# Optimization experiments

Measured on AMD Instinct MI355X. Metric: run time of the kernel, lower is better.

Reference implementation:

```python
import jax, jax.numpy as jnp
import numpy as np

B, S, HID = 8, 1024, 1024
NH, HD = 16, 64  # num heads, head dim
EPS = 1e-12


def setup_inputs() -> dict:
    key = jax.random.key(0)
    ks = jax.random.split(key, 8)
    sc = 0.02
    return {
        "hidden_states": jax.random.normal(ks[0], (B, S, HID), jnp.float32),
        "attention_mask": jnp.zeros((B, 1, 1, S), jnp.bool_),
        "rel_pos": jax.random.normal(ks[1], (1, NH, S, S), jnp.float32),
        "rel_2d_pos": jax.random.normal(ks[2], (1, NH, S, S), jnp.float32),
        "w_qkv": jax.random.normal(ks[3], (3 * HID, HID), jnp.float32) * sc,
        "q_bias": jnp.zeros((1, 1, HID), jnp.float32),
        "v_bias": jnp.zeros((1, 1, HID), jnp.float32),
        "w_out": jax.random.normal(ks[4], (HID, HID), jnp.float32) * sc,
        "b_out": jnp.zeros((HID,), jnp.float32),
        "ln_gamma": jnp.ones((HID,), jnp.float32),
        "ln_beta": jnp.zeros((HID,), jnp.float32),
    }


def reference(hidden_states, attention_mask, rel_pos, rel_2d_pos,
              w_qkv, q_bias, v_bias, w_out, b_out, ln_gamma, ln_beta):
    x = hidden_states
    # fast_qkv: single projection, no bias; then add q_bias/v_bias
    qkv = jnp.einsum('bsh,oh->bso', x, w_qkv)  # [B,S,3*HID]
    q, k, v = jnp.split(qkv, 3, axis=-1)
    q = q + q_bias
    v = v + v_bias
    # [B,S,HID] -> [B,NH,S,HD]
    to_heads = lambda t: t.reshape(B, S, NH, HD).transpose(0, 2, 1, 3)
    qh, kh, vh = to_heads(q), to_heads(k), to_heads(v)
    qh = qh / jnp.sqrt(jnp.float32(HD))
    scores = jnp.einsum('bhqd,bhkd->bhqk', qh, kh)
    scores = scores + rel_pos + rel_2d_pos
    scores = jnp.where(attention_mask, -jnp.inf, scores.astype(jnp.float32))
    probs = jax.nn.softmax(scores, axis=-1).astype(vh.dtype)
    ctx = jnp.einsum('bhqk,bhkd->bhqd', probs, vh)
    ctx = ctx.transpose(0, 2, 1, 3).reshape(B, S, HID)
    # self-output: dense + residual + LayerNorm
    h = jnp.einsum('bsh,oh->bso', ctx, w_out) + b_out + x
    mu = jnp.mean(h, axis=-1, keepdims=True)
    var = jnp.var(h, axis=-1, keepdims=True)
    out = (h - mu) / jnp.sqrt(var + EPS) * ln_gamma + ln_beta
    return out
```

## Files before the change

kernel.cpp:

```cpp
#include <hip/hip_runtime.h>
#include <stdint.h>
#include <stddef.h>

typedef unsigned short u16;
typedef __attribute__((ext_vector_type(8))) short short8;
typedef __attribute__((ext_vector_type(4))) float f32x4;
typedef __attribute__((ext_vector_type(4))) unsigned short ushort4v;
typedef __attribute__((ext_vector_type(4))) unsigned char uchar4v;
typedef __attribute__((ext_vector_type(2))) unsigned int uint2v;

constexpr int B_ = 8, S_ = 1024, HID_ = 1024, NH_ = 16, HD_ = 64;
#define LOG2E_F 1.4426950408889634f
#define QSCALE_F 0.18033688011112043f
#define SHIFT2_F 11.541560327111707f

__device__ __forceinline__ u16 f2b(float f) {
  unsigned int u = __builtin_bit_cast(unsigned int, f);
  u += 0x7fff + ((u >> 16) & 1);
  return (u16)(u >> 16);
}
__device__ __forceinline__ float b2f(u16 s) {
  unsigned int u = ((unsigned int)s) << 16;
  return __builtin_bit_cast(float, u);
}
__device__ __forceinline__ float fexp2(float x) {
#if __has_builtin(__builtin_amdgcn_exp2f)
  return __builtin_amdgcn_exp2f(x);
#else
  return exp2f(x);
#endif
}
__device__ __forceinline__ void llds16(const void* g, void* l) {
  __builtin_amdgcn_global_load_lds((__attribute__((address_space(1))) void*)g,
                                   (__attribute__((address_space(3))) void*)l, 16, 0, 0);
}

__global__ __launch_bounds__(256) void prep_cvt(
    const float* __restrict__ x, const float* __restrict__ wqkv,
    const float* __restrict__ wout, u16* __restrict__ xb,
    u16* __restrict__ wqkvb, u16* __restrict__ woutb) {
  const int NX4 = B_ * S_ * HID_ / 4, NW14 = 3 * HID_ * HID_ / 4, NW24 = HID_ * HID_ / 4;
  const int tot = NX4 + NW14 + NW24;
  for (int i = blockIdx.x * blockDim.x + threadIdx.x; i < tot; i += gridDim.x * blockDim.x) {
    const float4* s; u16* d; int j;
    if (i < NX4)              { s = (const float4*)x;    d = xb;    j = i; }
    else if (i < NX4 + NW14)  { s = (const float4*)wqkv; d = wqkvb; j = i - NX4; }
    else                      { s = (const float4*)wout; d = woutb; j = i - NX4 - NW14; }
    float4 v = s[j];
    ushort4v o; o[0] = f2b(v.x); o[1] = f2b(v.y); o[2] = f2b(v.z); o[3] = f2b(v.w);
    *(ushort4v*)(d + 4 * (size_t)j) = o;
  }
}

__global__ __launch_bounds__(256) void rel_perm(
    const float* __restrict__ a, const float* __restrict__ b, u16* __restrict__ relb) {
  __shared__ u16 lbuf[16 * 1032];
  const int qtg = blockIdx.x, h = blockIdx.y;
  const int t = threadIdx.x;
#pragma unroll
  for (int it = 0; it < 16; ++it) {
    int idx = it * 256 + t;
    int lq = idx >> 8, kc = idx & 255;
    size_t src = ((size_t)h * S_ + qtg * 16 + lq) * S_ + kc * 4;
    float4 va = *(const float4*)(a + src);
    float4 vb = *(const float4*)(b + src);
    ushort4v o;
    o[0] = f2b((va.x + vb.x) * LOG2E_F); o[1] = f2b((va.y + vb.y) * LOG2E_F);
    o[2] = f2b((va.z + vb.z) * LOG2E_F); o[3] = f2b((va.w + vb.w) * LOG2E_F);
    *(ushort4v*)(lbuf + lq * 1032 + kc * 4) = o;
  }
  __syncthreads();
#pragma unroll
  for (int it = 0; it < 16; ++it) {
    int c = it * 16 + (t >> 4);
    int ktg = c >> 2, qk = c & 3, lq = t & 15;
    ushort4v v = *(const ushort4v*)(lbuf + lq * 1032 + ktg * 16 + qk * 4);
    *(ushort4v*)(relb + ((((size_t)h * 64 + ktg) * 64 + qtg) * 4 + qk) * 64 + lq * 4) = v;
  }
}

__global__ __launch_bounds__(256) void gemm_qkv(
    const u16* __restrict__ W, const u16* __restrict__ X,
    const float* __restrict__ qbias, const float* __restrict__ vbias,
    u16* __restrict__ Qb, u16* __restrict__ Kb, u16* __restrict__ Vtb) {
  constexpr int K = HID_;
  __shared__ u16 smem[128 * 136];
  u16* Ws0 = smem;
  u16* Ws1 = smem + 4096;
  u16* Xs0 = smem + 8192;
  u16* Xs1 = smem + 12288;
  const int lin = blockIdx.x;
  const int virt = (lin & 7) * 192 + (lin >> 3);
  const int o0 = (virt % 24) * 128, s0 = (virt / 24) * 128;
  const int t = threadIdx.x, lane = t & 63, wv = t >> 6;
  const int wr = wv >> 1, wc = wv & 1, ln = lane & 15, q8 = lane >> 4;
  f32x4 acc[4][4] = {};

  for (int kt = 0; kt < K / 64; ++kt) {
    const int k0 = kt * 64;
#pragma unroll
    for (int c = 0; c < 2; ++c) {
      int idx = c * 256 + t, row = idx >> 2, cc = (idx & 3) * 8;
      const int db = (c * 256 + wv * 64) * 8;
      llds16(W + (size_t)(o0 + row) * K + k0 + cc,      Ws0 + db);
      llds16(W + (size_t)(o0 + row) * K + k0 + 32 + cc, Ws1 + db);
      llds16(X + (size_t)(s0 + row) * K + k0 + cc,      Xs0 + db);
      llds16(X + (size_t)(s0 + row) * K + k0 + 32 + cc, Xs1 + db);
    }
    __syncthreads();
#pragma unroll
    for (int hh = 0; hh < 2; ++hh) {
      const u16* Wh = hh ? Ws1 : Ws0;
      const u16* Xh = hh ? Xs1 : Xs0;
      short8 of[4], sf[4];
#pragma unroll
      for (int mi = 0; mi < 4; ++mi)
        of[mi] = *(const short8*)(Wh + (wr * 64 + mi * 16 + ln) * 32 + q8 * 8);
#pragma unroll
      for (int ni = 0; ni < 4; ++ni)
        sf[ni] = *(const short8*)(Xh + (wc * 64 + ni * 16 + ln) * 32 + q8 * 8);
#pragma unroll
      for (int mi = 0; mi < 4; ++mi)
#pragma unroll
        for (int ni = 0; ni < 4; ++ni)
          acc[mi][ni] = __builtin_amdgcn_mfma_f32_16x16x32_bf16(of[mi], sf[ni], acc[mi][ni], 0, 0, 0);
    }
    __syncthreads();
  }

  const int sec = o0 >> 10;

  if (sec == 2) {
#pragma unroll
    for (int mi = 0; mi < 4; ++mi) {
      const int ocol = wr * 64 + mi * 16 + q8 * 4;
      const int oo = (o0 + ocol) & 1023;
      float4 b4 = *(const float4*)(vbias + oo);
#pragma unroll
      for (int ni = 0; ni < 4; ++ni) {
        const int srow = wc * 64 + ni * 16 + ln;
#pragma unroll
        for (int r = 0; r < 4; ++r)
          smem[(ocol + r) * 136 + srow] = f2b(acc[mi][ni][r] + ((const float*)&b4)[r]);
      }
    }
    __syncthreads();
#pragma unroll
    for (int i = 0; i < 8; ++i) {
      int flat = i * 256 + t;
      int dl = flat >> 4, s8 = (flat & 15) * 8;
      short8 v = *(const short8*)(smem + dl * 136 + s8);
      int oo = (o0 + dl) & 1023, hh = oo >> 6, dd = oo & 63;
      int bb = s0 >> 10, ss = (s0 + s8) & 1023;
      *(short8*)(Vtb + ((size_t)(bb * NH_ + hh) * HD_ + dd) * S_ + ss) = v;
    }
    return;
  }

#pragma unroll
  for (int mi = 0; mi < 4; ++mi) {
    const int ocol = wr * 64 + mi * 16 + q8 * 4;
    const int oo = (o0 + ocol) & 1023;
    float4 b4;
    if (sec == 0) b4 = *(const float4*)(qbias + oo);
    else          b4 = float4{0.f, 0.f, 0.f, 0.f};
#pragma unroll
    for (int ni = 0; ni < 4; ++ni) {
      const int srow = wc * 64 + ni * 16 + ln;
      u16 e[4];
#pragma unroll
      for (int r = 0; r < 4; ++r) {
        float v = acc[mi][ni][r] + ((const float*)&b4)[r];
        if (sec == 0) v *= QSCALE_F;
        e[r] = f2b(v);
      }
      uint2v pw;
      pw[0] = (unsigned)e[0] | ((unsigned)e[1] << 16);
      pw[1] = (unsigned)e[2] | ((unsigned)e[3] << 16);
      *(uint2v*)(smem + srow * 136 + ocol) = pw;
    }
  }
  __syncthreads();
  u16* dst = (sec == 0) ? Qb : Kb;
#pragma unroll
  for (int i = 0; i < 8; ++i) {
    int flat = i * 256 + t;
    int srow = flat >> 4, c8 = (flat & 15) * 8;
    short8 v = *(const short8*)(smem + srow * 136 + c8);
    int oo = (o0 + c8) & 1023, hh = oo >> 6, dd = oo & 63;
    int s = s0 + srow, bb = s >> 10, ss = s & 1023;
    *(short8*)(dst + ((size_t)(bb * NH_ + hh) * S_ + ss) * HD_ + dd) = v;
  }
}

__global__ __launch_bounds__(512, 2) void flash_attn(
    const u16* __restrict__ Qb, const u16* __restrict__ Kb,
    const u16* __restrict__ Vtb, const u16* __restrict__ relb,
    const unsigned char* __restrict__ mask, u16* __restrict__ ctxb) {
  const int lin = blockIdx.x;
  const int virt = (lin & 7) * 64 + (lin >> 3);
  const int h = virt >> 5, qt_blk = (virt >> 3) & 3, b = virt & 7;
  const int bh = b * NH_ + h, q0 = qt_blk * 256;
  const int t = threadIdx.x, lane = t & 63, wv = t >> 6;
  const int ln = lane & 15, q8 = lane >> 4;

  __shared__ u16 smem[28160];
  u16* Ks  = smem;
  u16* Vts = smem + 9216;
  u16* Pw  = smem + 17920 + wv * 1280;

  const int krow = t >> 3, kcol = (t & 7) * 8;
  const int vrow = t >> 4, vcol = (t & 15) * 8;

  const u16* relbase = relb + (((size_t)h * 64) * 64 + (size_t)(qt_blk * 16 + wv * 2)) * 4 * 64
                            + (size_t)q8 * 64 + ln * 4;

  short8 kreg[2], vreg[2];
#pragma unroll
  for (int i = 0; i < 2; ++i)
    kreg[i] = *(const short8*)(Kb + ((size_t)bh * S_ + i * 64 + krow) * HD_ + kcol);
#pragma unroll
  for (int i = 0; i < 2; ++i)
    vreg[i] = *(const short8*)(Vtb + ((size_t)bh * HD_ + i * 32 + vrow) * S_ + vcol);

  short8 qf[2][2];
#pragma unroll
  for (int qt = 0; qt < 2; ++qt)
#pragma unroll
    for (int kc = 0; kc < 2; ++kc)
      qf[qt][kc] = *(const short8*)(Qb + ((size_t)bh * S_ + q0 + wv * 32 + qt * 16 + ln) * HD_ + kc * 32 + q8 * 8);

  f32x4 Oa[4][2] = {};
  float rs2[2] = {0.f, 0.f};

  for (int kt128 = 0; kt128 < 8; ++kt128) {
    const int k0 = kt128 * 128;

    uchar4v mg[4][2];
#pragma unroll
    for (int kvc = 0; kvc < 4; ++kvc)
#pragma unroll
      for (int sub = 0; sub < 2; ++sub)
        mg[kvc][sub] = *(const uchar4v*)(mask + b * S_ + k0 + (kvc * 2 + sub) * 16 + q8 * 4);

    ushort4v relg[4][2][2];
#pragma unroll
    for (int sub = 0; sub < 2; ++sub)
#pragma unroll
      for (int qt = 0; qt < 2; ++qt)
        relg[0][sub][qt] = *(const ushort4v*)(relbase +
            (((size_t)(kt128 * 8 + sub) * 64 + qt) * 4) * 64);

    __syncthreads();
#pragma unroll
    for (int i = 0; i < 2; ++i)
      *(short8*)(Ks + (i * 64 + krow) * 72 + kcol) = kreg[i];
#pragma unroll
    for (int i = 0; i < 2; ++i)
      *(short8*)(Vts + (i * 32 + vrow) * 136 + vcol) = vreg[i];
    if (kt128 < 7) {
      const int k0n = k0 + 128;
#pragma unroll
      for (int i = 0; i < 2; ++i)
        kreg[i] = *(const short8*)(Kb + ((size_t)bh * S_ + k0n + i * 64 + krow) * HD_ + kcol);
#pragma unroll
      for (int i = 0; i < 2; ++i)
        vreg[i] = *(const short8*)(Vtb + ((size_t)bh * HD_ + i * 32 + vrow) * S_ + k0n + vcol);
    }
    __syncthreads();

#pragma unroll
    for (int kvc = 0; kvc < 4; ++kvc) {
      if (kvc < 3) {
#pragma unroll
        for (int sub = 0; sub < 2; ++sub)
#pragma unroll
          for (int qt = 0; qt < 2; ++qt)
            relg[kvc + 1][sub][qt] = *(const ushort4v*)(relbase +
                (((size_t)(kt128 * 8 + (kvc + 1) * 2 + sub) * 64 + qt) * 4) * 64);
      }
#pragma unroll
      for (int sub = 0; sub < 2; ++sub) {
        const int kt = kvc * 2 + sub;
        short8 kf0 = *(const short8*)(Ks + (kt * 16 + ln) * 72 + q8 * 8);
        short8 kf1 = *(const short8*)(Ks + (kt * 16 + ln) * 72 + 32 + q8 * 8);
        uchar4v m4 = mg[kvc][sub];
        f32x4 mbase;
#pragma unroll
        for (int r = 0; r < 4; ++r) mbase[r] = (m4[r] ? -1e30f : 0.f) - SHIFT2_F;
#pragma unroll
        for (int qt = 0; qt < 2; ++qt) {
          ushort4v r4 = relg[kvc][sub][qt];
          f32x4 sc;
#pragma unroll
          for (int r = 0; r < 4; ++r) sc[r] = b2f(r4[r]) + mbase[r];
          sc = __builtin_amdgcn_mfma_f32_16x16x32_bf16(kf0, qf[qt][0], sc, 0, 0, 0);
          sc = __builtin_amdgcn_mfma_f32_16x16x32_bf16(kf1, qf[qt][1], sc, 0, 0, 0);
          float p0 = fexp2(sc[0]), p1 = fexp2(sc[1]);
          float p2 = fexp2(sc[2]), p3 = fexp2(sc[3]);
          rs2[qt] += (p0 + p1) + (p2 + p3);
          uint2v pw;
          pw[0] = (unsigned)f2b(p0) | ((unsigned)f2b(p1) << 16);
          pw[1] = (unsigned)f2b(p2) | ((unsigned)f2b(p3) << 16);
          *(uint2v*)(Pw + (qt * 16 + ln) * 40 + sub * 16 + q8 * 4) = pw;
        }
      }
      short8 pf0 = *(const short8*)(Pw + ln * 40 + q8 * 8);
      short8 pf1 = *(const short8*)(Pw + (16 + ln) * 40 + q8 * 8);
#pragma unroll
      for (int mt = 0; mt < 4; ++mt) {
        short8 vf = *(const short8*)(Vts + (mt * 16 + ln) * 136 + kvc * 32 + q8 * 8);
        Oa[mt][0] = __builtin_amdgcn_mfma_f32_16x16x32_bf16(vf, pf0, Oa[mt][0], 0, 0, 0);
        Oa[mt][1] = __builtin_amdgcn_mfma_f32_16x16x32_bf16(vf, pf1, Oa[mt][1], 0, 0, 0);
      }
    }
  }

  float inv[2];
#pragma unroll
  for (int qt = 0; qt < 2; ++qt) {
    rs2[qt] += __shfl_xor(rs2[qt], 16, 64);
    rs2[qt] += __shfl_xor(rs2[qt], 32, 64);
    inv[qt] = 1.f / rs2[qt];
  }

  __syncthreads();
  u16* Ob = smem + wv * 2304;
#pragma unroll
  for (int qt = 0; qt < 2; ++qt)
#pragma unroll
    for (int mt = 0; mt < 4; ++mt) {
      u16 e[4];
#pragma unroll
      for (int r = 0; r < 4; ++r) e[r] = f2b(Oa[mt][qt][r] * inv[qt]);
      uint2v pw;
      pw[0] = (unsigned)e[0] | ((unsigned)e[1] << 16);
      pw[1] = (unsigned)e[2] | ((unsigned)e[3] << 16);
      *(uint2v*)(Ob + (qt * 16 + ln) * 72 + mt * 16 + q8 * 4) = pw;
    }
#pragma unroll
  for (int p = 0; p < 4; ++p) {
    int row = p * 8 + (lane >> 3);
    int c8 = (lane & 7) * 8;
    short8 v = *(const short8*)(Ob + row * 72 + c8);
    int q = q0 + wv * 32 + row;
    *(short8*)(ctxb + ((size_t)(b * S_ + q)) * HID_ + h * 64 + c8) = v;
  }
}

__global__ __launch_bounds__(256) void gemm_out(
    const u16* __restrict__ W, const u16* __restrict__ X,
    const float* __restrict__ bout, const float* __restrict__ xres,
    u16* __restrict__ hb) {
  constexpr int K = HID_;
  __shared__ u16 smem[128 * 136];
  u16* Ws0 = smem;
  u16* Ws1 = smem + 4096;
  u16* Xs0 = smem + 8192;
  u16* Xs1 = smem + 12288;
  const int lin = blockIdx.x;
  const int virt = (lin & 7) * 64 + (lin >> 3);
  const int o0 = (virt % 8) * 128, s0 = (virt / 8) * 128;
  const int t = threadIdx.x, lane = t & 63, wv = t >> 6;
  const int wr = wv >> 1, wc = wv & 1, ln = lane & 15, q8 = lane >> 4;
  f32x4 acc[4][4] = {};

  for (int kt = 0; kt < K / 64; ++kt) {
    const int k0 = kt * 64;
#pragma unroll
    for (int c = 0; c < 2; ++c) {
      int idx = c * 256 + t, row = idx >> 2, cc = (idx & 3) * 8;
      const int db = (c * 256 + wv * 64) * 8;
      llds16(W + (size_t)(o0 + row) * K + k0 + cc,      Ws0 + db);
      llds16(W + (size_t)(o0 + row) * K + k0 + 32 + cc, Ws1 + db);
      llds16(X + (size_t)(s0 + row) * K + k0 + cc,      Xs0 + db);
      llds16(X + (size_t)(s0 + row) * K + k0 + 32 + cc, Xs1 + db);
    }
    __syncthreads();
#pragma unroll
    for (int hh = 0; hh < 2; ++hh) {
      const u16* Wh = hh ? Ws1 : Ws0;
      const u16* Xh = hh ? Xs1 : Xs0;
      short8 of[4], sf[4];
#pragma unroll
      for (int mi = 0; mi < 4; ++mi)
        of[mi] = *(const short8*)(Wh + (wr * 64 + mi * 16 + ln) * 32 + q8 * 8);
#pragma unroll
      for (int ni = 0; ni < 4; ++ni)
        sf[ni] = *(const short8*)(Xh + (wc * 64 + ni * 16 + ln) * 32 + q8 * 8);
#pragma unroll
      for (int mi = 0; mi < 4; ++mi)
#pragma unroll
        for (int ni = 0; ni < 4; ++ni)
          acc[mi][ni] = __builtin_amdgcn_mfma_f32_16x16x32_bf16(of[mi], sf[ni], acc[mi][ni], 0, 0, 0);
    }
    __syncthreads();
  }

#pragma unroll
  for (int mi = 0; mi < 4; ++mi) {
    const int ocol = wr * 64 + mi * 16 + q8 * 4;
    float4 b4 = *(const float4*)(bout + o0 + ocol);
#pragma unroll
    for (int ni = 0; ni < 4; ++ni) {
      const int srow = wc * 64 + ni * 16 + ln;
      u16 e[4];
#pragma unroll
      for (int r = 0; r < 4; ++r) e[r] = f2b(acc[mi][ni][r] + ((const float*)&b4)[r]);
      uint2v pw;
      pw[0] = (unsigned)e[0] | ((unsigned)e[1] << 16);
      pw[1] = (unsigned)e[2] | ((unsigned)e[3] << 16);
      *(uint2v*)(smem + srow * 136 + ocol) = pw;
    }
  }
  __syncthreads();
#pragma unroll
  for (int i = 0; i < 8; ++i) {
    int flat = i * 256 + t;
    int srow = flat >> 4, c8 = (flat & 15) * 8;
    short8 v = *(const short8*)(smem + srow * 136 + c8);
    int s = s0 + srow, o = o0 + c8;
    float4 x0 = *(const float4*)(xres + (size_t)s * HID_ + o);
    float4 x1 = *(const float4*)(xres + (size_t)s * HID_ + o + 4);
    short8 st;
#pragma unroll
    for (int j = 0; j < 4; ++j) st[j] = (short)f2b(b2f((u16)v[j]) + ((const float*)&x0)[j]);
#pragma unroll
    for (int j = 0; j < 4; ++j) st[4 + j] = (short)f2b(b2f((u16)v[4 + j]) + ((const float*)&x1)[j]);
    *(short8*)(hb + (size_t)s * HID_ + o) = st;
  }
}

__global__ __launch_bounds__(256) void ln_kernel(
    const u16* __restrict__ hb, const float* __restrict__ gamma,
    const float* __restrict__ beta, float* __restrict__ out) {
  const int lane = threadIdx.x & 63, wv = threadIdx.x >> 6;
  const int row = blockIdx.x * 4 + wv;
  const u16* hr = hb + (size_t)row * HID_;
  float v[16];
  short8 a = *(const short8*)(hr + lane * 16);
  short8 c = *(const short8*)(hr + lane * 16 + 8);
#pragma unroll
  for (int j = 0; j < 8; ++j) { v[j] = b2f((u16)a[j]); v[8 + j] = b2f((u16)c[j]); }
  float sum = 0.f, sq = 0.f;
#pragma unroll
  for (int j = 0; j < 16; ++j) { sum += v[j]; sq += v[j] * v[j]; }
#pragma unroll
  for (int off = 1; off < 64; off <<= 1) {
    sum += __shfl_xor(sum, off, 64);
    sq  += __shfl_xor(sq, off, 64);
  }
  const float mu = sum * (1.f / HID_);
  const float var = sq * (1.f / HID_) - mu * mu;
  const float inv = 1.f / sqrtf(var + 1e-12f);
#pragma unroll
  for (int j = 0; j < 16; ++j) {
    const int n = lane * 16 + j;
    out[(size_t)row * HID_ + n] = (v[j] - mu) * inv * gamma[n] + beta[n];
  }
}

extern "C" void kernel_launch(void* const* d_in, const int* in_sizes, int n_in,
                              void* d_out, int out_size, void* d_ws, size_t ws_size,
                              hipStream_t stream) {
  (void)in_sizes; (void)n_in; (void)out_size; (void)ws_size;
  const float* x     = (const float*)d_in[0];
  const unsigned char* mask = (const unsigned char*)d_in[1];
  const float* relp  = (const float*)d_in[2];
  const float* rel2  = (const float*)d_in[3];
  const float* wqkv  = (const float*)d_in[4];
  const float* qbias = (const float*)d_in[5];
  const float* vbias = (const float*)d_in[6];
  const float* wout  = (const float*)d_in[7];
  const float* bout  = (const float*)d_in[8];
  const float* gamma = (const float*)d_in[9];
  const float* beta  = (const float*)d_in[10];
  float* out = (float*)d_out;

  char* ws = (char*)d_ws;
  const size_t MB = (size_t)1 << 20;
  u16* xb    = (u16*)(ws + 0 * MB);
  u16* wqkvb = (u16*)(ws + 16 * MB);
  u16* woutb = (u16*)(ws + 22 * MB);
  u16* relb  = (u16*)(ws + 24 * MB);
  u16* Qb    = (u16*)(ws + 56 * MB);
  u16* Kb    = (u16*)(ws + 72 * MB);
  u16* Vtb   = (u16*)(ws + 88 * MB);
  u16* ctxb  = (u16*)(ws + 104 * MB);
  u16* hb    = (u16*)(ws + 120 * MB);

  prep_cvt<<<1024, 256, 0, stream>>>(x, wqkv, wout, xb, wqkvb, woutb);
  rel_perm<<<dim3(64, 16), 256, 0, stream>>>(relp, rel2, relb);
  gemm_qkv<<<1536, 256, 0, stream>>>(wqkvb, xb, qbias, vbias, Qb, Kb, Vtb);
  flash_attn<<<512, 512, 0, stream>>>(Qb, Kb, Vtb, relb, mask, ctxb);
  gemm_out<<<512, 256, 0, stream>>>(woutb, ctxb, bout, x, hb);
  ln_kernel<<<2048, 256, 0, stream>>>(hb, gamma, beta, out);
}
```

Baseline: 399.9 us.

## Fuse rel-pos bias into attention; widen conversion and LayerNorm vector accesses

Drops the separate rel_perm kernel, which summed, scaled and permuted the two fp32 relative-position tensors into a bf16 buffer. Flash attention now reads both fp32 rel tensors directly per tile and adds them in registers, removing one launch and a write/read round trip. The cost is that each attention block now reads two fp32 tensors (about 4x the bytes of the bf16 permuted layout), and reused across the 8 batches, the rel data is read 8 times, with a less coalesced per-row access pattern and no prefetch. prep_cvt is changed to convert 8 elements per thread. ln_kernel is changed to one row per block with float4 stores and a shared-memory reduction.

```diff
diff --git a/kernel.cpp b/kernel.cpp
--- a/kernel.cpp
+++ b/kernel.cpp
@@ -39,43 +39,20 @@
     const float* __restrict__ x, const float* __restrict__ wqkv,
     const float* __restrict__ wout, u16* __restrict__ xb,
     u16* __restrict__ wqkvb, u16* __restrict__ woutb) {
-  const int NX4 = B_ * S_ * HID_ / 4, NW14 = 3 * HID_ * HID_ / 4, NW24 = HID_ * HID_ / 4;
-  const int tot = NX4 + NW14 + NW24;
+  const int NX8 = B_ * S_ * HID_ / 8, NW18 = 3 * HID_ * HID_ / 8, NW28 = HID_ * HID_ / 8;
+  const int tot = NX8 + NW18 + NW28;
   for (int i = blockIdx.x * blockDim.x + threadIdx.x; i < tot; i += gridDim.x * blockDim.x) {
     const float4* s; u16* d; int j;
-    if (i < NX4)              { s = (const float4*)x;    d = xb;    j = i; }
-    else if (i < NX4 + NW14)  { s = (const float4*)wqkv; d = wqkvb; j = i - NX4; }
-    else                      { s = (const float4*)wout; d = woutb; j = i - NX4 - NW14; }
-    float4 v = s[j];
-    ushort4v o; o[0] = f2b(v.x); o[1] = f2b(v.y); o[2] = f2b(v.z); o[3] = f2b(v.w);
-    *(ushort4v*)(d + 4 * (size_t)j) = o;
-  }
-}
-
-__global__ __launch_bounds__(256) void rel_perm(
-    const float* __restrict__ a, const float* __restrict__ b, u16* __restrict__ relb) {
-  __shared__ u16 lbuf[16 * 1032];
-  const int qtg = blockIdx.x, h = blockIdx.y;
-  const int t = threadIdx.x;
-#pragma unroll
-  for (int it = 0; it < 16; ++it) {
-    int idx = it * 256 + t;
-    int lq = idx >> 8, kc = idx & 255;
-    size_t src = ((size_t)h * S_ + qtg * 16 + lq) * S_ + kc * 4;
-    float4 va = *(const float4*)(a + src);
-    float4 vb = *(const float4*)(b + src);
-    ushort4v o;
-    o[0] = f2b((va.x + vb.x) * LOG2E_F); o[1] = f2b((va.y + vb.y) * LOG2E_F);
-    o[2] = f2b((va.z + vb.z) * LOG2E_F); o[3] = f2b((va.w + vb.w) * LOG2E_F);
-    *(ushort4v*)(lbuf + lq * 1032 + kc * 4) = o;
-  }
-  __syncthreads();
-#pragma unroll
-  for (int it = 0; it < 16; ++it) {
-    int c = it * 16 + (t >> 4);
-    int ktg = c >> 2, qk = c & 3, lq = t & 15;
-    ushort4v v = *(const ushort4v*)(lbuf + lq * 1032 + ktg * 16 + qk * 4);
-    *(ushort4v*)(relb + ((((size_t)h * 64 + ktg) * 64 + qtg) * 4 + qk) * 64 + lq * 4) = v;
+    if (i < NX8)              { s = (const float4*)x;    d = xb;    j = i; }
+    else if (i < NX8 + NW18)  { s = (const float4*)wqkv; d = wqkvb; j = i - NX8; }
+    else                      { s = (const float4*)wout; d = woutb; j = i - NX8 - NW18; }
+    float4 v0 = s[2 * (size_t)j], v1 = s[2 * (size_t)j + 1];
+    short8 o;
+    o[0] = (short)f2b(v0.x); o[1] = (short)f2b(v0.y);
+    o[2] = (short)f2b(v0.z); o[3] = (short)f2b(v0.w);
+    o[4] = (short)f2b(v1.x); o[5] = (short)f2b(v1.y);
+    o[6] = (short)f2b(v1.z); o[7] = (short)f2b(v1.w);
+    *(short8*)(d + 8 * (size_t)j) = o;
   }
 }
 
@@ -195,7 +172,8 @@
 
 __global__ __launch_bounds__(512, 2) void flash_attn(
     const u16* __restrict__ Qb, const u16* __restrict__ Kb,
-    const u16* __restrict__ Vtb, const u16* __restrict__ relb,
+    const u16* __restrict__ Vtb, const float* __restrict__ relp,
+    const float* __restrict__ rel2,
     const unsigned char* __restrict__ mask, u16* __restrict__ ctxb) {
   const int lin = blockIdx.x;
   const int virt = (lin & 7) * 64 + (lin >> 3);
@@ -212,8 +190,8 @@
   const int krow = t >> 3, kcol = (t & 7) * 8;
   const int vrow = t >> 4, vcol = (t & 15) * 8;
 
-  const u16* relbase = relb + (((size_t)h * 64) * 64 + (size_t)(qt_blk * 16 + wv * 2)) * 4 * 64
-                            + (size_t)q8 * 64 + ln * 4;
+  const float* relA = relp + ((size_t)h * S_ + q0 + wv * 32 + ln) * S_;
+  const float* relB = rel2 + ((size_t)h * S_ + q0 + wv * 32 + ln) * S_;
 
   short8 kreg[2], vreg[2];
 #pragma unroll
@@ -242,14 +220,6 @@
 #pragma unroll
       for (int sub = 0; sub < 2; ++sub)
         mg[kvc][sub] = *(const uchar4v*)(mask + b * S_ + k0 + (kvc * 2 + sub) * 16 + q8 * 4);
-
-    ushort4v relg[4][2][2];
-#pragma unroll
-    for (int sub = 0; sub < 2; ++sub)
-#pragma unroll
-      for (int qt = 0; qt < 2; ++qt)
-        relg[0][sub][qt] = *(const ushort4v*)(relbase +
-            (((size_t)(kt128 * 8 + sub) * 64 + qt) * 4) * 64);
 
     __syncthreads();
 #pragma unroll
@@ -271,17 +241,10 @@
 
 #pragma unroll
     for (int kvc = 0; kvc < 4; ++kvc) {
-      if (kvc < 3) {
-#pragma unroll
-        for (int sub = 0; sub < 2; ++sub)
-#pragma unroll
-          for (int qt = 0; qt < 2; ++qt)
-            relg[kvc + 1][sub][qt] = *(const ushort4v*)(relbase +
-                (((size_t)(kt128 * 8 + (kvc + 1) * 2 + sub) * 64 + qt) * 4) * 64);
-      }
 #pragma unroll
       for (int sub = 0; sub < 2; ++sub) {
         const int kt = kvc * 2 + sub;
+        const int kg = k0 + kt * 16 + q8 * 4;
         short8 kf0 = *(const short8*)(Ks + (kt * 16 + ln) * 72 + q8 * 8);
         short8 kf1 = *(const short8*)(Ks + (kt * 16 + ln) * 72 + 32 + q8 * 8);
         uchar4v m4 = mg[kvc][sub];
@@ -290,10 +253,13 @@
         for (int r = 0; r < 4; ++r) mbase[r] = (m4[r] ? -1e30f : 0.f) - SHIFT2_F;
 #pragma unroll
         for (int qt = 0; qt < 2; ++qt) {
-          ushort4v r4 = relg[kvc][sub][qt];
+          float4 ra = *(const float4*)(relA + (size_t)(qt * 16) * S_ + kg);
+          float4 rb = *(const float4*)(relB + (size_t)(qt * 16) * S_ + kg);
           f32x4 sc;
-#pragma unroll
-          for (int r = 0; r < 4; ++r) sc[r] = b2f(r4[r]) + mbase[r];
+          sc[0] = (ra.x + rb.x) * LOG2E_F + mbase[0];
+          sc[1] = (ra.y + rb.y) * LOG2E_F + mbase[1];
+          sc[2] = (ra.z + rb.z) * LOG2E_F + mbase[2];
+          sc[3] = (ra.w + rb.w) * LOG2E_F + mbase[3];
           sc = __builtin_amdgcn_mfma_f32_16x16x32_bf16(kf0, qf[qt][0], sc, 0, 0, 0);
           sc = __builtin_amdgcn_mfma_f32_16x16x32_bf16(kf1, qf[qt][1], sc, 0, 0, 0);
           float p0 = fexp2(sc[0]), p1 = fexp2(sc[1]);
@@ -434,30 +400,36 @@
 __global__ __launch_bounds__(256) void ln_kernel(
     const u16* __restrict__ hb, const float* __restrict__ gamma,
     const float* __restrict__ beta, float* __restrict__ out) {
-  const int lane = threadIdx.x & 63, wv = threadIdx.x >> 6;
-  const int row = blockIdx.x * 4 + wv;
+  __shared__ float red[8];
+  const int t = threadIdx.x, lane = t & 63, wv = t >> 6;
+  const int row = blockIdx.x;
   const u16* hr = hb + (size_t)row * HID_;
-  float v[16];
-  short8 a = *(const short8*)(hr + lane * 16);
-  short8 c = *(const short8*)(hr + lane * 16 + 8);
-#pragma unroll
-  for (int j = 0; j < 8; ++j) { v[j] = b2f((u16)a[j]); v[8 + j] = b2f((u16)c[j]); }
-  float sum = 0.f, sq = 0.f;
-#pragma unroll
-  for (int j = 0; j < 16; ++j) { sum += v[j]; sq += v[j] * v[j]; }
+  ushort4v a = *(const ushort4v*)(hr + t * 4);
+  float v[4];
+#pragma unroll
+  for (int j = 0; j < 4; ++j) v[j] = b2f(a[j]);
+  float sum = (v[0] + v[1]) + (v[2] + v[3]);
+  float sq = (v[0] * v[0] + v[1] * v[1]) + (v[2] * v[2] + v[3] * v[3]);
 #pragma unroll
   for (int off = 1; off < 64; off <<= 1) {
     sum += __shfl_xor(sum, off, 64);
     sq  += __shfl_xor(sq, off, 64);
   }
-  const float mu = sum * (1.f / HID_);
-  const float var = sq * (1.f / HID_) - mu * mu;
+  if (lane == 0) { red[wv] = sum; red[4 + wv] = sq; }
+  __syncthreads();
+  const float s4 = (red[0] + red[1]) + (red[2] + red[3]);
+  const float q4 = (red[4] + red[5]) + (red[6] + red[7]);
+  const float mu = s4 * (1.f / HID_);
+  const float var = q4 * (1.f / HID_) - mu * mu;
   const float inv = 1.f / sqrtf(var + 1e-12f);
-#pragma unroll
-  for (int j = 0; j < 16; ++j) {
-    const int n = lane * 16 + j;
-    out[(size_t)row * HID_ + n] = (v[j] - mu) * inv * gamma[n] + beta[n];
-  }
+  float4 g = *(const float4*)(gamma + t * 4);
+  float4 be = *(const float4*)(beta + t * 4);
+  float4 o;
+  o.x = (v[0] - mu) * inv * g.x + be.x;
+  o.y = (v[1] - mu) * inv * g.y + be.y;
+  o.z = (v[2] - mu) * inv * g.z + be.z;
+  o.w = (v[3] - mu) * inv * g.w + be.w;
+  *(float4*)(out + (size_t)row * HID_ + t * 4) = o;
 }
 
 extern "C" void kernel_launch(void* const* d_in, const int* in_sizes, int n_in,
@@ -482,17 +454,15 @@
   u16* xb    = (u16*)(ws + 0 * MB);
   u16* wqkvb = (u16*)(ws + 16 * MB);
   u16* woutb = (u16*)(ws + 22 * MB);
-  u16* relb  = (u16*)(ws + 24 * MB);
   u16* Qb    = (u16*)(ws + 56 * MB);
   u16* Kb    = (u16*)(ws + 72 * MB);
   u16* Vtb   = (u16*)(ws + 88 * MB);
   u16* ctxb  = (u16*)(ws + 104 * MB);
   u16* hb    = (u16*)(ws + 120 * MB);
 
-  prep_cvt<<<1024, 256, 0, stream>>>(x, wqkv, wout, xb, wqkvb, woutb);
-  rel_perm<<<dim3(64, 16), 256, 0, stream>>>(relp, rel2, relb);
+  prep_cvt<<<2048, 256, 0, stream>>>(x, wqkv, wout, xb, wqkvb, woutb);
   gemm_qkv<<<1536, 256, 0, stream>>>(wqkvb, xb, qbias, vbias, Qb, Kb, Vtb);
-  flash_attn<<<512, 512, 0, stream>>>(Qb, Kb, Vtb, relb, mask, ctxb);
+  flash_attn<<<512, 512, 0, stream>>>(Qb, Kb, Vtb, relp, rel2, mask, ctxb);
   gemm_out<<<512, 256, 0, stream>>>(woutb, ctxb, bout, x, hb);
-  ln_kernel<<<2048, 256, 0, stream>>>(hb, gamma, beta, out);
-}
+  ln_kernel<<<8192, 256, 0, stream>>>(hb, gamma, beta, out);
+}
```

Result: slower. 447.8 us (+12.0%).
